# Optimization experiments

Hardware: AMD Instinct MI355X
Metric: run time of the kernel (lower is better)

Reference implementation:

```python
import jax, jax.numpy as jnp
import numpy as np

EPS = 1e-6


def setup_inputs() -> dict:
    key = jax.random.key(0)
    k1, k2 = jax.random.split(key)
    B, Lq, Lk, D = 16, 1024, 1024, 512
    query = jax.random.normal(k1, (B, Lq, D), dtype=jnp.float32)
    context = jax.random.normal(k2, (B, Lk, D), dtype=jnp.float32)
    gamma = jnp.ones((D,), dtype=jnp.float32)
    beta = jnp.zeros((D,), dtype=jnp.float32)
    return {"query": query, "context": context, "gamma": gamma, "beta": beta}


def _layer_norm(x, gamma, beta):
    mean = jnp.mean(x, axis=-1, keepdims=True)
    var = jnp.var(x, axis=-1, keepdims=True)
    return gamma * (x - mean) * jax.lax.rsqrt(var + EPS) + beta


def reference(query, context, gamma, beta):
    # query: [B, Lq, D], context: [B, Lk, D]
    D = query.shape[-1]
    scale = 1.0 / np.sqrt(D).astype(np.float32)
    # additive-style tanh-activated scores: [B, Lq, Lk]
    score = jnp.tanh(jnp.einsum('bqd,bkd->bqk', query, context) * scale)
    attn = jax.nn.softmax(score, axis=2)
    # dropout is identity in eval/reference mode
    out = jnp.einsum('bqk,bkd->bqd', attn, context)
    out = _layer_norm(out + query, gamma, beta)
    return out
```

## Files before the change

kernel.cpp:

```cpp
#include <hip/hip_runtime.h>
#include <hip/hip_bf16.h>
#include <cstdint>

#define LQ 1024
#define LK 1024
#define DD 512
#define NB 16
#define QB 64
#define KB 32
#define NT (LK / KB)
#define CSTRIDE 1088
#define CSZ (32 * CSTRIDE)
#define PSZ (64 * 80)

typedef short bf16x8 __attribute__((ext_vector_type(8)));
typedef float f32x4 __attribute__((ext_vector_type(4)));

__device__ __forceinline__ uint16_t f2bf(float f) {
  uint32_t u = __builtin_bit_cast(uint32_t, f);
  u = (u + 0x7fffu + ((u >> 16) & 1u)) >> 16;
  return (uint16_t)u;
}

__device__ __forceinline__ void load_lds16(const void* g, void* l) {
  __builtin_amdgcn_global_load_lds(
      (const __attribute__((address_space(1))) uint32_t*)g,
      (__attribute__((address_space(3))) uint32_t*)l, 16, 0, 0);
}

__global__ __launch_bounds__(256) void prep_kernel(const float* __restrict__ c,
                                                   uint16_t* __restrict__ cb,
                                                   uint16_t* __restrict__ ct) {
  __shared__ float t[32][33];
  const int k0 = blockIdx.x * 32, d0 = blockIdx.y * 32, b = blockIdx.z;
  const float* src = c + (size_t)b * LK * DD;
  uint16_t* cbd = cb + (size_t)b * LK * DD;
  uint16_t* ctd = ct + (size_t)b * DD * LK;
  const int tx = threadIdx.x, ty = threadIdx.y;
  for (int j = 0; j < 4; ++j) {
    int k = ty + j * 8;
    float v = src[(size_t)(k0 + k) * DD + d0 + tx];
    t[k][tx] = v;
    cbd[(size_t)(k0 + k) * DD + d0 + tx] = f2bf(v);
  }
  __syncthreads();
  for (int j = 0; j < 4; ++j) {
    int d = ty + j * 8;
    ctd[(size_t)(d0 + d) * LK + k0 + tx] = f2bf(t[tx][d]);
  }
}

__global__ __launch_bounds__(512, 2) void attn_kernel(
    const uint16_t* __restrict__ Cb, const uint16_t* __restrict__ Ctb,
    const float* __restrict__ Qf, const float* __restrict__ gamma,
    const float* __restrict__ beta, float* __restrict__ out) {
  __shared__ uint4 cs4[3 * CSZ / 16];
  __shared__ char plds[3 * PSZ];
  __shared__ float denom_s[64];
  __shared__ float rsum_s[64], rsumsq_s[64], mean_s[64], rstd_s[64];

  const int tid = threadIdx.x;
  const int w = tid >> 6, l = tid & 63, c = l & 15, g = l >> 4;
  const int orig = blockIdx.x;
  const int virt = ((orig & 7) << 5) | (orig >> 3);
  const int b = virt >> 4, qblk = virt & 15;
  const int q0 = qblk * QB;
  const int mt = w & 1, qt = w >> 1;
  const float scale = 0.044194173824159216f;

  if (tid < 64) { denom_s[tid] = 0.f; rsum_s[tid] = 0.f; rsumsq_s[tid] = 0.f; }

  bf16x8 qfrag[16];
  {
    const float* qrow = Qf + ((size_t)b * LQ + q0 + qt * 16 + c) * DD;
    for (int s = 0; s < 16; ++s) {
      float4 a0 = *(const float4*)(qrow + s * 32 + g * 8);
      float4 a1 = *(const float4*)(qrow + s * 32 + g * 8 + 4);
      ushort4 u0, u1;
      u0.x = f2bf(a0.x); u0.y = f2bf(a0.y); u0.z = f2bf(a0.z); u0.w = f2bf(a0.w);
      u1.x = f2bf(a1.x); u1.y = f2bf(a1.y); u1.z = f2bf(a1.z); u1.w = f2bf(a1.w);
      union { ushort4 u[2]; bf16x8 v; } pk;
      pk.u[0] = u0; pk.u[1] = u1;
      qfrag[s] = pk.v;
    }
  }

  const int kkA = mt * 16 + c;
  const int aoff = kkA * CSTRIDE + ((g ^ (kkA & 3)) * 16);

  f32x4 oacc[4][4];
  for (int i = 0; i < 4; ++i)
    for (int j = 0; j < 4; ++j) oacc[i][j] = (f32x4){0.f, 0.f, 0.f, 0.f};
  float dacc = 0.f;

  const char* cbyte = (const char*)Cb + (size_t)b * LK * DD * 2;
  const char* ctbyte = (const char*)Ctb + (size_t)b * DD * LK * 2;

  int csrcoff[4];
  for (int j = 0; j < 4; ++j) {
    int r = w * 4 + j;
    csrcoff[j] = r * 1024 + ((l * 16) ^ ((r & 3) << 4));
  }
  const char* pbbase = ctbyte + (size_t)(w * 64 + c) * 2048 + g * 16;

  char* cs0 = (char*)cs4;
  char* cs1 = cs0 + CSZ;
  char* cs2 = cs1 + CSZ;
  char* pl0 = plds;
  char* pl1 = pl0 + PSZ;
  char* pl2 = pl1 + PSZ;
  const int pwoff = (qt * 16 + c) * 80 + (mt * 16 + g * 4) * 2;
  const int proff = c * 80 + g * 16;

  auto stageC = [&](char* dst, int kt2) {
    const char* s0 = cbyte + (size_t)kt2 * 32768;
    for (int j = 0; j < 4; ++j)
      load_lds16(s0 + csrcoff[j], dst + (w * 4 + j) * CSTRIDE);
  };
  auto loadPB = [&](bf16x8(&pbn)[4], int kt2) {
    const char* p = pbbase + kt2 * 64;
    pbn[0] = *(const bf16x8*)(p);
    pbn[1] = *(const bf16x8*)(p + 32768);
    pbn[2] = *(const bf16x8*)(p + 65536);
    pbn[3] = *(const bf16x8*)(p + 98304);
  };

  bf16x8 pbX[4], pbY[4], pbZ[4];

  stageC(cs0, 0);
  stageC(cs1, 1);
  __syncthreads();

  auto body = [&](int kt, const char* csR, char* csW, const char* pR, char* pW,
                  bf16x8(&pbc)[4], bf16x8(&pbn)[4], bool doStage, bool doPV) {
    if (doStage) stageC(csW, kt + 2);
    loadPB(pbn, kt);
    if (doPV) {
      bf16x8 pa[4];
      for (int q2 = 0; q2 < 4; ++q2) pa[q2] = *(const bf16x8*)(pR + proff + q2 * 1280);
      __builtin_amdgcn_s_setprio(1);
      for (int q2 = 0; q2 < 4; ++q2)
        for (int n2 = 0; n2 < 4; ++n2)
          oacc[q2][n2] =
              __builtin_amdgcn_mfma_f32_16x16x32_bf16(pa[q2], pbc[n2], oacc[q2][n2], 0, 0, 0);
      __builtin_amdgcn_s_setprio(0);
    }
    f32x4 s0v = {0.f, 0.f, 0.f, 0.f}, s1v = {0.f, 0.f, 0.f, 0.f};
    {
      const char* ar = csR + aoff;
      __builtin_amdgcn_s_setprio(1);
      for (int s = 0; s < 8; ++s) {
        bf16x8 a0 = *(const bf16x8*)(ar + s * 64);
        bf16x8 a1 = *(const bf16x8*)(ar + (s + 8) * 64);
        s0v = __builtin_amdgcn_mfma_f32_16x16x32_bf16(a0, qfrag[s], s0v, 0, 0, 0);
        s1v = __builtin_amdgcn_mfma_f32_16x16x32_bf16(a1, qfrag[s + 8], s1v, 0, 0, 0);
      }
      __builtin_amdgcn_s_setprio(0);
    }
    {
      float pv[4];
      for (int i = 0; i < 4; ++i) {
        float sv = (s0v[i] + s1v[i]) * scale;
        float e2 = __expf(sv * 2.f);
        float r = __builtin_amdgcn_rcpf(e2 + 1.f);
        float th = (e2 - 1.f) * r;
        float p = __expf(th);
        pv[i] = p;
        dacc += p;
      }
      uint2 pk;
      pk.x = ((uint32_t)f2bf(pv[1]) << 16) | f2bf(pv[0]);
      pk.y = ((uint32_t)f2bf(pv[3]) << 16) | f2bf(pv[2]);
      *(uint2*)(pW + pwoff) = pk;
    }
    asm volatile("s_waitcnt lgkmcnt(0)" ::: "memory");
    __builtin_amdgcn_s_barrier();
    __builtin_amdgcn_sched_barrier(0);
  };

  for (int kt = 0; kt < NT - 2; kt += 3) {
    body(kt,     cs0, cs2, pl2, pl0, pbZ, pbX, kt + 2 < NT, kt > 0);
    body(kt + 1, cs1, cs0, pl0, pl1, pbX, pbY, kt + 3 < NT, true);
    body(kt + 2, cs2, cs1, pl1, pl2, pbY, pbZ, kt + 4 < NT, true);
  }
  body(NT - 2, cs0, cs2, pl2, pl0, pbZ, pbX, false, true);
  body(NT - 1, cs1, cs0, pl0, pl1, pbX, pbY, false, true);
  {
    bf16x8 pa[4];
    for (int q2 = 0; q2 < 4; ++q2) pa[q2] = *(const bf16x8*)(pl1 + proff + q2 * 1280);
    for (int q2 = 0; q2 < 4; ++q2)
      for (int n2 = 0; n2 < 4; ++n2)
        oacc[q2][n2] =
            __builtin_amdgcn_mfma_f32_16x16x32_bf16(pa[q2], pbY[n2], oacc[q2][n2], 0, 0, 0);
  }

  float dv = dacc;
  dv += __shfl_xor(dv, 16);
  dv += __shfl_xor(dv, 32);
  if (l < 16) atomicAdd(&denom_s[qt * 16 + l], dv);
  __syncthreads();

  const float* qsrc = Qf + ((size_t)b * LQ + q0) * DD;
  for (int q2 = 0; q2 < 4; ++q2)
    for (int i = 0; i < 4; ++i) {
      int row = q2 * 16 + g * 4 + i;
      float inv = 1.f / denom_s[row];
      for (int nt = 0; nt < 4; ++nt) {
        int d = w * 64 + nt * 16 + c;
        float o = oacc[q2][nt][i] * inv + qsrc[(size_t)row * DD + d];
        oacc[q2][nt][i] = o;
      }
    }
  for (int q2 = 0; q2 < 4; ++q2)
    for (int i = 0; i < 4; ++i) {
      float s1 = 0.f, s2 = 0.f;
      for (int nt = 0; nt < 4; ++nt) {
        float v = oacc[q2][nt][i];
        s1 += v;
        s2 += v * v;
      }
      s1 += __shfl_xor(s1, 1); s2 += __shfl_xor(s2, 1);
      s1 += __shfl_xor(s1, 2); s2 += __shfl_xor(s2, 2);
      s1 += __shfl_xor(s1, 4); s2 += __shfl_xor(s2, 4);
      s1 += __shfl_xor(s1, 8); s2 += __shfl_xor(s2, 8);
      if (c == 0) {
        int row = q2 * 16 + g * 4 + i;
        atomicAdd(&rsum_s[row], s1);
        atomicAdd(&rsumsq_s[row], s2);
      }
    }
  __syncthreads();
  if (tid < 64) {
    float m = rsum_s[tid] * (1.f / DD);
    float var = rsumsq_s[tid] * (1.f / DD) - m * m;
    mean_s[tid] = m;
    rstd_s[tid] = rsqrtf(fmaxf(var, 0.f) + 1e-6f);
  }
  __syncthreads();
  float* op = out + ((size_t)b * LQ + q0) * DD;
  for (int q2 = 0; q2 < 4; ++q2)
    for (int i = 0; i < 4; ++i) {
      int row = q2 * 16 + g * 4 + i;
      float m = mean_s[row], r = rstd_s[row];
      for (int nt = 0; nt < 4; ++nt) {
        int d = w * 64 + nt * 16 + c;
        op[(size_t)row * DD + d] = gamma[d] * ((oacc[q2][nt][i] - m) * r) + beta[d];
      }
    }
}

__global__ __launch_bounds__(256) void naive_kernel(const float* __restrict__ Q,
                                                    const float* __restrict__ C,
                                                    const float* __restrict__ gamma,
                                                    const float* __restrict__ beta,
                                                    float* __restrict__ out) {
  const int row = blockIdx.x;
  const int b = row >> 10;
  const int tid = threadIdx.x;
  __shared__ float qs[DD];
  __shared__ float ps[LK];
  __shared__ float ys[DD];
  __shared__ float red[256];
  const float* qp = Q + (size_t)row * DD;
  const float* cb = C + (size_t)b * LK * DD;
  for (int d = tid; d < DD; d += 256) qs[d] = qp[d];
  __syncthreads();
  for (int k = tid; k < LK; k += 256) {
    const float* cr = cb + (size_t)k * DD;
    float s = 0.f;
    for (int d = 0; d < DD; ++d) s += qs[d] * cr[d];
    s *= 0.044194173824159216f;
    float e2 = __expf(2.f * s);
    float th = (e2 - 1.f) / (e2 + 1.f);
    ps[k] = __expf(th);
  }
  __syncthreads();
  float dsum = 0.f;
  for (int k = tid; k < LK; k += 256) dsum += ps[k];
  red[tid] = dsum;
  __syncthreads();
  for (int off = 128; off; off >>= 1) {
    if (tid < off) red[tid] += red[tid + off];
    __syncthreads();
  }
  float inv = 1.f / red[0];
  __syncthreads();
  for (int d = tid; d < DD; d += 256) {
    float o = 0.f;
    for (int k = 0; k < LK; ++k) o += ps[k] * cb[(size_t)k * DD + d];
    ys[d] = o * inv + qs[d];
  }
  __syncthreads();
  float s1 = 0.f;
  for (int d = tid; d < DD; d += 256) s1 += ys[d];
  red[tid] = s1;
  __syncthreads();
  for (int off = 128; off; off >>= 1) {
    if (tid < off) red[tid] += red[tid + off];
    __syncthreads();
  }
  float mean = red[0] * (1.f / DD);
  __syncthreads();
  float s2 = 0.f;
  for (int d = tid; d < DD; d += 256) {
    float v = ys[d] - mean;
    s2 += v * v;
  }
  red[tid] = s2;
  __syncthreads();
  for (int off = 128; off; off >>= 1) {
    if (tid < off) red[tid] += red[tid + off];
    __syncthreads();
  }
  float rstd = rsqrtf(red[0] * (1.f / DD) + 1e-6f);
  for (int d = tid; d < DD; d += 256)
    out[(size_t)row * DD + d] = gamma[d] * ((ys[d] - mean) * rstd) + beta[d];
}

extern "C" void kernel_launch(void* const* d_in, const int* in_sizes, int n_in,
                              void* d_out, int out_size, void* d_ws, size_t ws_size,
                              hipStream_t stream) {
  const float* Qf = (const float*)d_in[0];
  const float* Cf = (const float*)d_in[1];
  const float* gamma = (const float*)d_in[2];
  const float* beta = (const float*)d_in[3];
  float* out = (float*)d_out;
  const size_t nelem = (size_t)NB * LK * DD;
  const size_t need = nelem * 2 * 2;
  if (ws_size >= need) {
    uint16_t* Cb = (uint16_t*)d_ws;
    uint16_t* Ctb = Cb + nelem;
    prep_kernel<<<dim3(LK / 32, DD / 32, NB), dim3(32, 8), 0, stream>>>(Cf, Cb, Ctb);
    attn_kernel<<<256, 512, 0, stream>>>(Cb, Ctb, Qf, gamma, beta, out);
  } else {
    naive_kernel<<<NB * LQ, 256, 0, stream>>>(Qf, Cf, gamma, beta, out);
  }
}
```

Before: 96.15 us.

## Halve query block to 32 rows with 256-thread blocks and double buffering

Cuts the query tile from 64 to 32 rows, uses 4 waves per block instead of 8, and launches 512 blocks instead of 256 so more of the chip's compute units get work. Each wave now owns 128 output columns, with 8 PV accumulators per query subtile. The C staging pipeline drops from triple to double buffering, and the hand-placed waitcnt plus barrier is replaced by __syncthreads. The cost is that each K/V tile is reused across half as many query rows, so global traffic for the context doubles, and the shallower pipeline may expose more load latency.

```diff
diff --git a/kernel.cpp b/kernel.cpp
--- a/kernel.cpp
+++ b/kernel.cpp
@@ -6,12 +6,12 @@
 #define LK 1024
 #define DD 512
 #define NB 16
-#define QB 64
+#define QB 32
 #define KB 32
 #define NT (LK / KB)
 #define CSTRIDE 1088
 #define CSZ (32 * CSTRIDE)
-#define PSZ (64 * 80)
+#define PSZ (QB * 80)
 
 typedef short bf16x8 __attribute__((ext_vector_type(8)));
 typedef float f32x4 __attribute__((ext_vector_type(4)));
@@ -50,25 +50,25 @@
   }
 }
 
-__global__ __launch_bounds__(512, 2) void attn_kernel(
+__global__ __launch_bounds__(256, 2) void attn_kernel(
     const uint16_t* __restrict__ Cb, const uint16_t* __restrict__ Ctb,
     const float* __restrict__ Qf, const float* __restrict__ gamma,
     const float* __restrict__ beta, float* __restrict__ out) {
-  __shared__ uint4 cs4[3 * CSZ / 16];
-  __shared__ char plds[3 * PSZ];
-  __shared__ float denom_s[64];
-  __shared__ float rsum_s[64], rsumsq_s[64], mean_s[64], rstd_s[64];
+  __shared__ uint4 cs4[2 * CSZ / 16];
+  __shared__ char plds[2 * PSZ];
+  __shared__ float denom_s[QB];
+  __shared__ float rsum_s[QB], rsumsq_s[QB], mean_s[QB], rstd_s[QB];
 
   const int tid = threadIdx.x;
   const int w = tid >> 6, l = tid & 63, c = l & 15, g = l >> 4;
   const int orig = blockIdx.x;
-  const int virt = ((orig & 7) << 5) | (orig >> 3);
-  const int b = virt >> 4, qblk = virt & 15;
+  const int virt = ((orig & 7) << 6) | (orig >> 3);
+  const int b = virt >> 5, qblk = virt & 31;
   const int q0 = qblk * QB;
   const int mt = w & 1, qt = w >> 1;
   const float scale = 0.044194173824159216f;
 
-  if (tid < 64) { denom_s[tid] = 0.f; rsum_s[tid] = 0.f; rsumsq_s[tid] = 0.f; }
+  if (tid < QB) { denom_s[tid] = 0.f; rsum_s[tid] = 0.f; rsumsq_s[tid] = 0.f; }
 
   bf16x8 qfrag[16];
   {
@@ -88,66 +88,63 @@
   const int kkA = mt * 16 + c;
   const int aoff = kkA * CSTRIDE + ((g ^ (kkA & 3)) * 16);
 
-  f32x4 oacc[4][4];
-  for (int i = 0; i < 4; ++i)
-    for (int j = 0; j < 4; ++j) oacc[i][j] = (f32x4){0.f, 0.f, 0.f, 0.f};
+  f32x4 oacc[2][8];
+  for (int i = 0; i < 2; ++i)
+    for (int j = 0; j < 8; ++j) oacc[i][j] = (f32x4){0.f, 0.f, 0.f, 0.f};
   float dacc = 0.f;
 
   const char* cbyte = (const char*)Cb + (size_t)b * LK * DD * 2;
   const char* ctbyte = (const char*)Ctb + (size_t)b * DD * LK * 2;
 
-  int csrcoff[4];
-  for (int j = 0; j < 4; ++j) {
-    int r = w * 4 + j;
+  int csrcoff[8];
+  for (int j = 0; j < 8; ++j) {
+    int r = w * 8 + j;
     csrcoff[j] = r * 1024 + ((l * 16) ^ ((r & 3) << 4));
   }
-  const char* pbbase = ctbyte + (size_t)(w * 64 + c) * 2048 + g * 16;
+  const char* pbbase = ctbyte + (size_t)(w * 128 + c) * 2048 + g * 16;
 
   char* cs0 = (char*)cs4;
   char* cs1 = cs0 + CSZ;
-  char* cs2 = cs1 + CSZ;
   char* pl0 = plds;
   char* pl1 = pl0 + PSZ;
-  char* pl2 = pl1 + PSZ;
   const int pwoff = (qt * 16 + c) * 80 + (mt * 16 + g * 4) * 2;
   const int proff = c * 80 + g * 16;
 
   auto stageC = [&](char* dst, int kt2) {
     const char* s0 = cbyte + (size_t)kt2 * 32768;
-    for (int j = 0; j < 4; ++j)
-      load_lds16(s0 + csrcoff[j], dst + (w * 4 + j) * CSTRIDE);
+    for (int j = 0; j < 8; ++j)
+      load_lds16(s0 + csrcoff[j], dst + (w * 8 + j) * CSTRIDE);
   };
-  auto loadPB = [&](bf16x8(&pbn)[4], int kt2) {
+  auto loadPB = [&](bf16x8(&pbn)[8], int kt2) {
     const char* p = pbbase + kt2 * 64;
-    pbn[0] = *(const bf16x8*)(p);
-    pbn[1] = *(const bf16x8*)(p + 32768);
-    pbn[2] = *(const bf16x8*)(p + 65536);
-    pbn[3] = *(const bf16x8*)(p + 98304);
+    for (int nt = 0; nt < 8; ++nt)
+      pbn[nt] = *(const bf16x8*)(p + (size_t)nt * 32768);
   };
 
-  bf16x8 pbX[4], pbY[4], pbZ[4];
+  bf16x8 pbA[8], pbB[8];
 
   stageC(cs0, 0);
-  stageC(cs1, 1);
-  __syncthreads();
-
-  auto body = [&](int kt, const char* csR, char* csW, const char* pR, char* pW,
-                  bf16x8(&pbc)[4], bf16x8(&pbn)[4], bool doStage, bool doPV) {
-    if (doStage) stageC(csW, kt + 2);
+  __syncthreads();
+
+  auto body = [&](int kt, bf16x8(&pbc)[8], bf16x8(&pbn)[8]) {
+    const int cur = kt & 1;
+    if (kt + 1 < NT) stageC(cur ? cs0 : cs1, kt + 1);
     loadPB(pbn, kt);
-    if (doPV) {
-      bf16x8 pa[4];
-      for (int q2 = 0; q2 < 4; ++q2) pa[q2] = *(const bf16x8*)(pR + proff + q2 * 1280);
+    if (kt) {
+      const char* par = (cur ? pl0 : pl1) + proff;
+      bf16x8 pa[2];
+      pa[0] = *(const bf16x8*)(par);
+      pa[1] = *(const bf16x8*)(par + 1280);
       __builtin_amdgcn_s_setprio(1);
-      for (int q2 = 0; q2 < 4; ++q2)
-        for (int n2 = 0; n2 < 4; ++n2)
+      for (int q2 = 0; q2 < 2; ++q2)
+        for (int n2 = 0; n2 < 8; ++n2)
           oacc[q2][n2] =
               __builtin_amdgcn_mfma_f32_16x16x32_bf16(pa[q2], pbc[n2], oacc[q2][n2], 0, 0, 0);
       __builtin_amdgcn_s_setprio(0);
     }
     f32x4 s0v = {0.f, 0.f, 0.f, 0.f}, s1v = {0.f, 0.f, 0.f, 0.f};
     {
-      const char* ar = csR + aoff;
+      const char* ar = (cur ? cs1 : cs0) + aoff;
       __builtin_amdgcn_s_setprio(1);
       for (int s = 0; s < 8; ++s) {
         bf16x8 a0 = *(const bf16x8*)(ar + s * 64);
@@ -171,27 +168,23 @@
       uint2 pk;
       pk.x = ((uint32_t)f2bf(pv[1]) << 16) | f2bf(pv[0]);
       pk.y = ((uint32_t)f2bf(pv[3]) << 16) | f2bf(pv[2]);
-      *(uint2*)(pW + pwoff) = pk;
-    }
-    asm volatile("s_waitcnt lgkmcnt(0)" ::: "memory");
-    __builtin_amdgcn_s_barrier();
-    __builtin_amdgcn_sched_barrier(0);
+      *(uint2*)((cur ? pl1 : pl0) + pwoff) = pk;
+    }
+    __syncthreads();
   };
 
-  for (int kt = 0; kt < NT - 2; kt += 3) {
-    body(kt,     cs0, cs2, pl2, pl0, pbZ, pbX, kt + 2 < NT, kt > 0);
-    body(kt + 1, cs1, cs0, pl0, pl1, pbX, pbY, kt + 3 < NT, true);
-    body(kt + 2, cs2, cs1, pl1, pl2, pbY, pbZ, kt + 4 < NT, true);
-  }
-  body(NT - 2, cs0, cs2, pl2, pl0, pbZ, pbX, false, true);
-  body(NT - 1, cs1, cs0, pl0, pl1, pbX, pbY, false, true);
+  for (int kt = 0; kt < NT; kt += 2) {
+    body(kt, pbB, pbA);
+    body(kt + 1, pbA, pbB);
+  }
   {
-    bf16x8 pa[4];
-    for (int q2 = 0; q2 < 4; ++q2) pa[q2] = *(const bf16x8*)(pl1 + proff + q2 * 1280);
-    for (int q2 = 0; q2 < 4; ++q2)
-      for (int n2 = 0; n2 < 4; ++n2)
+    bf16x8 pa[2];
+    pa[0] = *(const bf16x8*)(pl1 + proff);
+    pa[1] = *(const bf16x8*)(pl1 + proff + 1280);
+    for (int q2 = 0; q2 < 2; ++q2)
+      for (int n2 = 0; n2 < 8; ++n2)
         oacc[q2][n2] =
-            __builtin_amdgcn_mfma_f32_16x16x32_bf16(pa[q2], pbY[n2], oacc[q2][n2], 0, 0, 0);
+            __builtin_amdgcn_mfma_f32_16x16x32_bf16(pa[q2], pbB[n2], oacc[q2][n2], 0, 0, 0);
   }
 
   float dv = dacc;
@@ -201,20 +194,20 @@
   __syncthreads();
 
   const float* qsrc = Qf + ((size_t)b * LQ + q0) * DD;
-  for (int q2 = 0; q2 < 4; ++q2)
+  for (int q2 = 0; q2 < 2; ++q2)
     for (int i = 0; i < 4; ++i) {
       int row = q2 * 16 + g * 4 + i;
       float inv = 1.f / denom_s[row];
-      for (int nt = 0; nt < 4; ++nt) {
-        int d = w * 64 + nt * 16 + c;
+      for (int nt = 0; nt < 8; ++nt) {
+        int d = w * 128 + nt * 16 + c;
         float o = oacc[q2][nt][i] * inv + qsrc[(size_t)row * DD + d];
         oacc[q2][nt][i] = o;
       }
     }
-  for (int q2 = 0; q2 < 4; ++q2)
+  for (int q2 = 0; q2 < 2; ++q2)
     for (int i = 0; i < 4; ++i) {
       float s1 = 0.f, s2 = 0.f;
-      for (int nt = 0; nt < 4; ++nt) {
+      for (int nt = 0; nt < 8; ++nt) {
         float v = oacc[q2][nt][i];
         s1 += v;
         s2 += v * v;
@@ -230,7 +223,7 @@
       }
     }
   __syncthreads();
-  if (tid < 64) {
+  if (tid < QB) {
     float m = rsum_s[tid] * (1.f / DD);
     float var = rsumsq_s[tid] * (1.f / DD) - m * m;
     mean_s[tid] = m;
@@ -238,12 +231,12 @@
   }
   __syncthreads();
   float* op = out + ((size_t)b * LQ + q0) * DD;
-  for (int q2 = 0; q2 < 4; ++q2)
+  for (int q2 = 0; q2 < 2; ++q2)
     for (int i = 0; i < 4; ++i) {
       int row = q2 * 16 + g * 4 + i;
       float m = mean_s[row], r = rstd_s[row];
-      for (int nt = 0; nt < 4; ++nt) {
-        int d = w * 64 + nt * 16 + c;
+      for (int nt = 0; nt < 8; ++nt) {
+        int d = w * 128 + nt * 16 + c;
         op[(size_t)row * DD + d] = gamma[d] * ((oacc[q2][nt][i] - m) * r) + beta[d];
       }
     }
@@ -331,7 +324,7 @@
     uint16_t* Cb = (uint16_t*)d_ws;
     uint16_t* Ctb = Cb + nelem;
     prep_kernel<<<dim3(LK / 32, DD / 32, NB), dim3(32, 8), 0, stream>>>(Cf, Cb, Ctb);
-    attn_kernel<<<256, 512, 0, stream>>>(Cb, Ctb, Qf, gamma, beta, out);
+    attn_kernel<<<512, 256, 0, stream>>>(Cb, Ctb, Qf, gamma, beta, out);
   } else {
     naive_kernel<<<NB * LQ, 256, 0, stream>>>(Qf, Cf, gamma, beta, out);
   }
```

Result: slower. 109.7 us (+14.1%).

## Warp-specialize attention kernel into score and PV producer/consumer warp groups

Applied to the files above, without the earlier changes.

Splits the 512-thread block into a 1024-thread block. Waves 0-7 compute QK scores, tanh and exp and write P tiles to double-buffered LDS. Waves 8-15 stage C tiles into LDS, load transposed C, run the PV MFMAs and do the layernorm epilogue. The aim is to overlap score computation with the PV matmul and global loads across separate waves rather than interleaving both in every wave. In exchange, occupancy drops to one block per CU. The barrier pairing between the two groups is subtle and a possible correctness risk, including the matched __syncthreads counts and the vmcnt wait covering the staged loads.

```diff
diff --git a/kernel.cpp b/kernel.cpp
--- a/kernel.cpp
+++ b/kernel.cpp
@@ -11,7 +11,7 @@
 #define NT (LK / KB)
 #define CSTRIDE 1088
 #define CSZ (32 * CSTRIDE)
-#define PSZ (64 * 80)
+#define PSZ (QB * 80)
 
 typedef short bf16x8 __attribute__((ext_vector_type(8)));
 typedef float f32x4 __attribute__((ext_vector_type(4)));
@@ -50,14 +50,14 @@
   }
 }
 
-__global__ __launch_bounds__(512, 2) void attn_kernel(
+__global__ __launch_bounds__(1024) void attn_kernel(
     const uint16_t* __restrict__ Cb, const uint16_t* __restrict__ Ctb,
     const float* __restrict__ Qf, const float* __restrict__ gamma,
     const float* __restrict__ beta, float* __restrict__ out) {
   __shared__ uint4 cs4[3 * CSZ / 16];
-  __shared__ char plds[3 * PSZ];
-  __shared__ float denom_s[64];
-  __shared__ float rsum_s[64], rsumsq_s[64], mean_s[64], rstd_s[64];
+  __shared__ char plds[2 * PSZ];
+  __shared__ float denom_s[QB];
+  __shared__ float rsum_s[QB], rsumsq_s[QB], mean_s[QB], rstd_s[QB];
 
   const int tid = threadIdx.x;
   const int w = tid >> 6, l = tid & 63, c = l & 15, g = l >> 4;
@@ -65,89 +65,60 @@
   const int virt = ((orig & 7) << 5) | (orig >> 3);
   const int b = virt >> 4, qblk = virt & 15;
   const int q0 = qblk * QB;
-  const int mt = w & 1, qt = w >> 1;
   const float scale = 0.044194173824159216f;
 
-  if (tid < 64) { denom_s[tid] = 0.f; rsum_s[tid] = 0.f; rsumsq_s[tid] = 0.f; }
-
-  bf16x8 qfrag[16];
-  {
-    const float* qrow = Qf + ((size_t)b * LQ + q0 + qt * 16 + c) * DD;
-    for (int s = 0; s < 16; ++s) {
-      float4 a0 = *(const float4*)(qrow + s * 32 + g * 8);
-      float4 a1 = *(const float4*)(qrow + s * 32 + g * 8 + 4);
-      ushort4 u0, u1;
-      u0.x = f2bf(a0.x); u0.y = f2bf(a0.y); u0.z = f2bf(a0.z); u0.w = f2bf(a0.w);
-      u1.x = f2bf(a1.x); u1.y = f2bf(a1.y); u1.z = f2bf(a1.z); u1.w = f2bf(a1.w);
-      union { ushort4 u[2]; bf16x8 v; } pk;
-      pk.u[0] = u0; pk.u[1] = u1;
-      qfrag[s] = pk.v;
-    }
-  }
-
-  const int kkA = mt * 16 + c;
-  const int aoff = kkA * CSTRIDE + ((g ^ (kkA & 3)) * 16);
-
-  f32x4 oacc[4][4];
-  for (int i = 0; i < 4; ++i)
-    for (int j = 0; j < 4; ++j) oacc[i][j] = (f32x4){0.f, 0.f, 0.f, 0.f};
-  float dacc = 0.f;
+  if (tid < QB) { denom_s[tid] = 0.f; rsum_s[tid] = 0.f; rsumsq_s[tid] = 0.f; }
 
   const char* cbyte = (const char*)Cb + (size_t)b * LK * DD * 2;
   const char* ctbyte = (const char*)Ctb + (size_t)b * DD * LK * 2;
-
-  int csrcoff[4];
-  for (int j = 0; j < 4; ++j) {
-    int r = w * 4 + j;
-    csrcoff[j] = r * 1024 + ((l * 16) ^ ((r & 3) << 4));
-  }
-  const char* pbbase = ctbyte + (size_t)(w * 64 + c) * 2048 + g * 16;
-
   char* cs0 = (char*)cs4;
   char* cs1 = cs0 + CSZ;
   char* cs2 = cs1 + CSZ;
   char* pl0 = plds;
-  char* pl1 = pl0 + PSZ;
-  char* pl2 = pl1 + PSZ;
-  const int pwoff = (qt * 16 + c) * 80 + (mt * 16 + g * 4) * 2;
-  const int proff = c * 80 + g * 16;
-
-  auto stageC = [&](char* dst, int kt2) {
-    const char* s0 = cbyte + (size_t)kt2 * 32768;
-    for (int j = 0; j < 4; ++j)
-      load_lds16(s0 + csrcoff[j], dst + (w * 4 + j) * CSTRIDE);
-  };
-  auto loadPB = [&](bf16x8(&pbn)[4], int kt2) {
-    const char* p = pbbase + kt2 * 64;
-    pbn[0] = *(const bf16x8*)(p);
-    pbn[1] = *(const bf16x8*)(p + 32768);
-    pbn[2] = *(const bf16x8*)(p + 65536);
-    pbn[3] = *(const bf16x8*)(p + 98304);
-  };
-
-  bf16x8 pbX[4], pbY[4], pbZ[4];
-
-  stageC(cs0, 0);
-  stageC(cs1, 1);
-  __syncthreads();
-
-  auto body = [&](int kt, const char* csR, char* csW, const char* pR, char* pW,
-                  bf16x8(&pbc)[4], bf16x8(&pbn)[4], bool doStage, bool doPV) {
-    if (doStage) stageC(csW, kt + 2);
-    loadPB(pbn, kt);
-    if (doPV) {
-      bf16x8 pa[4];
-      for (int q2 = 0; q2 < 4; ++q2) pa[q2] = *(const bf16x8*)(pR + proff + q2 * 1280);
-      __builtin_amdgcn_s_setprio(1);
-      for (int q2 = 0; q2 < 4; ++q2)
-        for (int n2 = 0; n2 < 4; ++n2)
-          oacc[q2][n2] =
-              __builtin_amdgcn_mfma_f32_16x16x32_bf16(pa[q2], pbc[n2], oacc[q2][n2], 0, 0, 0);
-      __builtin_amdgcn_s_setprio(0);
-    }
-    f32x4 s0v = {0.f, 0.f, 0.f, 0.f}, s1v = {0.f, 0.f, 0.f, 0.f};
+  char* pl1 = plds + PSZ;
+
+  const int cw = w - 8;
+  int csrcoff[4];
+  for (int j = 0; j < 4; ++j) {
+    int r = (cw & 7) * 4 + j;
+    csrcoff[j] = r * 1024 + ((l * 16) ^ ((r & 3) << 4));
+  }
+
+  if (w >= 8) {
+    const char* s0 = cbyte;
+    for (int j = 0; j < 4; ++j) {
+      load_lds16(s0 + csrcoff[j], cs0 + (cw * 4 + j) * CSTRIDE);
+      load_lds16(s0 + 32768 + csrcoff[j], cs1 + (cw * 4 + j) * CSTRIDE);
+    }
+  }
+  __syncthreads();
+
+  if (w < 8) {
+    const int mt = w & 1, qt = w >> 1;
+    bf16x8 qfrag[16];
     {
+      const float* qrow = Qf + ((size_t)b * LQ + q0 + qt * 16 + c) * DD;
+      for (int s = 0; s < 16; ++s) {
+        float4 a0 = *(const float4*)(qrow + s * 32 + g * 8);
+        float4 a1 = *(const float4*)(qrow + s * 32 + g * 8 + 4);
+        ushort4 u0, u1;
+        u0.x = f2bf(a0.x); u0.y = f2bf(a0.y); u0.z = f2bf(a0.z); u0.w = f2bf(a0.w);
+        u1.x = f2bf(a1.x); u1.y = f2bf(a1.y); u1.z = f2bf(a1.z); u1.w = f2bf(a1.w);
+        union { ushort4 u[2]; bf16x8 v; } pk;
+        pk.u[0] = u0; pk.u[1] = u1;
+        qfrag[s] = pk.v;
+      }
+    }
+    const int kkA = mt * 16 + c;
+    const int aoff = kkA * CSTRIDE + ((g ^ (kkA & 3)) * 16);
+    const int pwoff = (qt * 16 + c) * 80 + (mt * 16 + g * 4) * 2;
+    float dacc = 0.f;
+
+#pragma unroll
+    for (int kt = 0; kt < NT; ++kt) {
+      const char* csR = (kt % 3 == 0) ? cs0 : (kt % 3 == 1) ? cs1 : cs2;
       const char* ar = csR + aoff;
+      f32x4 s0v = {0.f, 0.f, 0.f, 0.f}, s1v = {0.f, 0.f, 0.f, 0.f};
       __builtin_amdgcn_s_setprio(1);
       for (int s = 0; s < 8; ++s) {
         bf16x8 a0 = *(const bf16x8*)(ar + s * 64);
@@ -156,8 +127,6 @@
         s1v = __builtin_amdgcn_mfma_f32_16x16x32_bf16(a1, qfrag[s + 8], s1v, 0, 0, 0);
       }
       __builtin_amdgcn_s_setprio(0);
-    }
-    {
       float pv[4];
       for (int i = 0; i < 4; ++i) {
         float sv = (s0v[i] + s1v[i]) * scale;
@@ -171,82 +140,122 @@
       uint2 pk;
       pk.x = ((uint32_t)f2bf(pv[1]) << 16) | f2bf(pv[0]);
       pk.y = ((uint32_t)f2bf(pv[3]) << 16) | f2bf(pv[2]);
-      *(uint2*)(pW + pwoff) = pk;
-    }
-    asm volatile("s_waitcnt lgkmcnt(0)" ::: "memory");
-    __builtin_amdgcn_s_barrier();
-    __builtin_amdgcn_sched_barrier(0);
-  };
-
-  for (int kt = 0; kt < NT - 2; kt += 3) {
-    body(kt,     cs0, cs2, pl2, pl0, pbZ, pbX, kt + 2 < NT, kt > 0);
-    body(kt + 1, cs1, cs0, pl0, pl1, pbX, pbY, kt + 3 < NT, true);
-    body(kt + 2, cs2, cs1, pl1, pl2, pbY, pbZ, kt + 4 < NT, true);
-  }
-  body(NT - 2, cs0, cs2, pl2, pl0, pbZ, pbX, false, true);
-  body(NT - 1, cs1, cs0, pl0, pl1, pbX, pbY, false, true);
-  {
-    bf16x8 pa[4];
-    for (int q2 = 0; q2 < 4; ++q2) pa[q2] = *(const bf16x8*)(pl1 + proff + q2 * 1280);
+      *(uint2*)(((kt & 1) ? pl1 : pl0) + pwoff) = pk;
+      asm volatile("s_waitcnt lgkmcnt(0)" ::: "memory");
+      __builtin_amdgcn_s_barrier();
+      __builtin_amdgcn_sched_barrier(0);
+    }
+    float dv = dacc;
+    dv += __shfl_xor(dv, 16);
+    dv += __shfl_xor(dv, 32);
+    if (l < 16) atomicAdd(&denom_s[qt * 16 + l], dv);
+  } else {
+    const char* pbbase = ctbyte + (size_t)(cw * 64 + c) * 2048 + g * 16;
+    const int proff = c * 80 + g * 16;
+    f32x4 oacc[4][4];
+    for (int i = 0; i < 4; ++i)
+      for (int j = 0; j < 4; ++j) oacc[i][j] = (f32x4){0.f, 0.f, 0.f, 0.f};
+    bf16x8 pb[4];
+
+#pragma unroll
+    for (int kt = 0; kt < NT; ++kt) {
+      if (kt > 0) {
+        const char* p = pbbase + (size_t)(kt - 1) * 64;
+        pb[0] = *(const bf16x8*)(p);
+        pb[1] = *(const bf16x8*)(p + 32768);
+        pb[2] = *(const bf16x8*)(p + 65536);
+        pb[3] = *(const bf16x8*)(p + 98304);
+      }
+      __builtin_amdgcn_sched_barrier(0);
+      if (kt + 2 < NT) {
+        char* csW = ((kt + 2) % 3 == 0) ? cs0 : ((kt + 2) % 3 == 1) ? cs1 : cs2;
+        const char* s0 = cbyte + (size_t)(kt + 2) * 32768;
+        for (int j = 0; j < 4; ++j)
+          load_lds16(s0 + csrcoff[j], csW + (cw * 4 + j) * CSTRIDE);
+      }
+      if (kt > 0) {
+        const char* par = ((kt & 1) ? pl0 : pl1) + proff;
+        bf16x8 pa[4];
+        for (int q2 = 0; q2 < 4; ++q2) pa[q2] = *(const bf16x8*)(par + q2 * 1280);
+        __builtin_amdgcn_s_setprio(1);
+        for (int q2 = 0; q2 < 4; ++q2)
+          for (int n2 = 0; n2 < 4; ++n2)
+            oacc[q2][n2] =
+                __builtin_amdgcn_mfma_f32_16x16x32_bf16(pa[q2], pb[n2], oacc[q2][n2], 0, 0, 0);
+        __builtin_amdgcn_s_setprio(0);
+      }
+      asm volatile("s_waitcnt vmcnt(8)" ::: "memory");
+      __builtin_amdgcn_s_barrier();
+      __builtin_amdgcn_sched_barrier(0);
+    }
+    {
+      const char* p = pbbase + (size_t)(NT - 1) * 64;
+      pb[0] = *(const bf16x8*)(p);
+      pb[1] = *(const bf16x8*)(p + 32768);
+      pb[2] = *(const bf16x8*)(p + 65536);
+      pb[3] = *(const bf16x8*)(p + 98304);
+      const char* par = pl1 + proff;
+      bf16x8 pa[4];
+      for (int q2 = 0; q2 < 4; ++q2) pa[q2] = *(const bf16x8*)(par + q2 * 1280);
+      for (int q2 = 0; q2 < 4; ++q2)
+        for (int n2 = 0; n2 < 4; ++n2)
+          oacc[q2][n2] =
+              __builtin_amdgcn_mfma_f32_16x16x32_bf16(pa[q2], pb[n2], oacc[q2][n2], 0, 0, 0);
+    }
+    __syncthreads();
+
+    const float* qsrc = Qf + ((size_t)b * LQ + q0) * DD;
     for (int q2 = 0; q2 < 4; ++q2)
-      for (int n2 = 0; n2 < 4; ++n2)
-        oacc[q2][n2] =
-            __builtin_amdgcn_mfma_f32_16x16x32_bf16(pa[q2], pbY[n2], oacc[q2][n2], 0, 0, 0);
-  }
-
-  float dv = dacc;
-  dv += __shfl_xor(dv, 16);
-  dv += __shfl_xor(dv, 32);
-  if (l < 16) atomicAdd(&denom_s[qt * 16 + l], dv);
-  __syncthreads();
-
-  const float* qsrc = Qf + ((size_t)b * LQ + q0) * DD;
-  for (int q2 = 0; q2 < 4; ++q2)
-    for (int i = 0; i < 4; ++i) {
-      int row = q2 * 16 + g * 4 + i;
-      float inv = 1.f / denom_s[row];
-      for (int nt = 0; nt < 4; ++nt) {
-        int d = w * 64 + nt * 16 + c;
-        float o = oacc[q2][nt][i] * inv + qsrc[(size_t)row * DD + d];
-        oacc[q2][nt][i] = o;
-      }
-    }
-  for (int q2 = 0; q2 < 4; ++q2)
-    for (int i = 0; i < 4; ++i) {
-      float s1 = 0.f, s2 = 0.f;
-      for (int nt = 0; nt < 4; ++nt) {
-        float v = oacc[q2][nt][i];
-        s1 += v;
-        s2 += v * v;
-      }
-      s1 += __shfl_xor(s1, 1); s2 += __shfl_xor(s2, 1);
-      s1 += __shfl_xor(s1, 2); s2 += __shfl_xor(s2, 2);
-      s1 += __shfl_xor(s1, 4); s2 += __shfl_xor(s2, 4);
-      s1 += __shfl_xor(s1, 8); s2 += __shfl_xor(s2, 8);
-      if (c == 0) {
+      for (int i = 0; i < 4; ++i) {
         int row = q2 * 16 + g * 4 + i;
-        atomicAdd(&rsum_s[row], s1);
-        atomicAdd(&rsumsq_s[row], s2);
-      }
-    }
-  __syncthreads();
-  if (tid < 64) {
+        float inv = 1.f / denom_s[row];
+        for (int nt = 0; nt < 4; ++nt) {
+          int d = cw * 64 + nt * 16 + c;
+          float o = oacc[q2][nt][i] * inv + qsrc[(size_t)row * DD + d];
+          oacc[q2][nt][i] = o;
+        }
+      }
+    for (int q2 = 0; q2 < 4; ++q2)
+      for (int i = 0; i < 4; ++i) {
+        float s1 = 0.f, s2 = 0.f;
+        for (int nt = 0; nt < 4; ++nt) {
+          float v = oacc[q2][nt][i];
+          s1 += v;
+          s2 += v * v;
+        }
+        s1 += __shfl_xor(s1, 1); s2 += __shfl_xor(s2, 1);
+        s1 += __shfl_xor(s1, 2); s2 += __shfl_xor(s2, 2);
+        s1 += __shfl_xor(s1, 4); s2 += __shfl_xor(s2, 4);
+        s1 += __shfl_xor(s1, 8); s2 += __shfl_xor(s2, 8);
+        if (c == 0) {
+          int row = q2 * 16 + g * 4 + i;
+          atomicAdd(&rsum_s[row], s1);
+          atomicAdd(&rsumsq_s[row], s2);
+        }
+      }
+    __syncthreads();
+    __syncthreads();
+    float* op = out + ((size_t)b * LQ + q0) * DD;
+    for (int q2 = 0; q2 < 4; ++q2)
+      for (int i = 0; i < 4; ++i) {
+        int row = q2 * 16 + g * 4 + i;
+        float m = mean_s[row], r = rstd_s[row];
+        for (int nt = 0; nt < 4; ++nt) {
+          int d = cw * 64 + nt * 16 + c;
+          op[(size_t)row * DD + d] = gamma[d] * ((oacc[q2][nt][i] - m) * r) + beta[d];
+        }
+      }
+    return;
+  }
+  __syncthreads();
+  __syncthreads();
+  if (tid < QB) {
     float m = rsum_s[tid] * (1.f / DD);
     float var = rsumsq_s[tid] * (1.f / DD) - m * m;
     mean_s[tid] = m;
     rstd_s[tid] = rsqrtf(fmaxf(var, 0.f) + 1e-6f);
   }
   __syncthreads();
-  float* op = out + ((size_t)b * LQ + q0) * DD;
-  for (int q2 = 0; q2 < 4; ++q2)
-    for (int i = 0; i < 4; ++i) {
-      int row = q2 * 16 + g * 4 + i;
-      float m = mean_s[row], r = rstd_s[row];
-      for (int nt = 0; nt < 4; ++nt) {
-        int d = w * 64 + nt * 16 + c;
-        op[(size_t)row * DD + d] = gamma[d] * ((oacc[q2][nt][i] - m) * r) + beta[d];
-      }
-    }
 }
 
 __global__ __launch_bounds__(256) void naive_kernel(const float* __restrict__ Q,
@@ -331,7 +340,7 @@
     uint16_t* Cb = (uint16_t*)d_ws;
     uint16_t* Ctb = Cb + nelem;
     prep_kernel<<<dim3(LK / 32, DD / 32, NB), dim3(32, 8), 0, stream>>>(Cf, Cb, Ctb);
-    attn_kernel<<<256, 512, 0, stream>>>(Cb, Ctb, Qf, gamma, beta, out);
+    attn_kernel<<<256, 1024, 0, stream>>>(Cb, Ctb, Qf, gamma, beta, out);
   } else {
     naive_kernel<<<NB * LQ, 256, 0, stream>>>(Qf, Cf, gamma, beta, out);
   }
```

New measurement: 100.9 us. 1.05x slower.

## Replace triple-buffered skewed pipeline with double-buffered two-barrier loop

Applied to the files above, without the earlier changes.

Replaces the 3-stage rotating LDS pipeline, where the P·V MFMA for tile kt-1 overlapped the score MFMA for tile kt, with a 2-buffer scheme. Each iteration computes scores, writes P to one LDS buffer, synchronizes, then does P·V in the same step, prefetching the next C tile and Ct fragments one step ahead. This cuts LDS usage, which may help occupancy, and registers for the extra PB buffer. In exchange it adds a second barrier per tile and loses the cross-tile overlap of the two MFMA phases.

```diff
diff --git a/kernel.cpp b/kernel.cpp
--- a/kernel.cpp
+++ b/kernel.cpp
@@ -11,7 +11,7 @@
 #define NT (LK / KB)
 #define CSTRIDE 1088
 #define CSZ (32 * CSTRIDE)
-#define PSZ (64 * 80)
+#define PSZ (QB * 80)
 
 typedef short bf16x8 __attribute__((ext_vector_type(8)));
 typedef float f32x4 __attribute__((ext_vector_type(4)));
@@ -54,10 +54,10 @@
     const uint16_t* __restrict__ Cb, const uint16_t* __restrict__ Ctb,
     const float* __restrict__ Qf, const float* __restrict__ gamma,
     const float* __restrict__ beta, float* __restrict__ out) {
-  __shared__ uint4 cs4[3 * CSZ / 16];
-  __shared__ char plds[3 * PSZ];
-  __shared__ float denom_s[64];
-  __shared__ float rsum_s[64], rsumsq_s[64], mean_s[64], rstd_s[64];
+  __shared__ uint4 cs4[2 * CSZ / 16];
+  __shared__ char plds[PSZ];
+  __shared__ float denom_s[QB];
+  __shared__ float rsum_s[QB], rsumsq_s[QB], mean_s[QB], rstd_s[QB];
 
   const int tid = threadIdx.x;
   const int w = tid >> 6, l = tid & 63, c = l & 15, g = l >> 4;
@@ -68,7 +68,7 @@
   const int mt = w & 1, qt = w >> 1;
   const float scale = 0.044194173824159216f;
 
-  if (tid < 64) { denom_s[tid] = 0.f; rsum_s[tid] = 0.f; rsumsq_s[tid] = 0.f; }
+  if (tid < QB) { denom_s[tid] = 0.f; rsum_s[tid] = 0.f; rsumsq_s[tid] = 0.f; }
 
   bf16x8 qfrag[16];
   {
@@ -105,10 +105,6 @@
 
   char* cs0 = (char*)cs4;
   char* cs1 = cs0 + CSZ;
-  char* cs2 = cs1 + CSZ;
-  char* pl0 = plds;
-  char* pl1 = pl0 + PSZ;
-  char* pl2 = pl1 + PSZ;
   const int pwoff = (qt * 16 + c) * 80 + (mt * 16 + g * 4) * 2;
   const int proff = c * 80 + g * 16;
 
@@ -118,32 +114,26 @@
       load_lds16(s0 + csrcoff[j], dst + (w * 4 + j) * CSTRIDE);
   };
   auto loadPB = [&](bf16x8(&pbn)[4], int kt2) {
-    const char* p = pbbase + kt2 * 64;
+    const char* p = pbbase + (size_t)kt2 * 64;
     pbn[0] = *(const bf16x8*)(p);
     pbn[1] = *(const bf16x8*)(p + 32768);
     pbn[2] = *(const bf16x8*)(p + 65536);
     pbn[3] = *(const bf16x8*)(p + 98304);
   };
 
-  bf16x8 pbX[4], pbY[4], pbZ[4];
+  bf16x8 pbA[4], pbB[4];
 
   stageC(cs0, 0);
-  stageC(cs1, 1);
-  __syncthreads();
-
-  auto body = [&](int kt, const char* csR, char* csW, const char* pR, char* pW,
-                  bf16x8(&pbc)[4], bf16x8(&pbn)[4], bool doStage, bool doPV) {
-    if (doStage) stageC(csW, kt + 2);
-    loadPB(pbn, kt);
-    if (doPV) {
-      bf16x8 pa[4];
-      for (int q2 = 0; q2 < 4; ++q2) pa[q2] = *(const bf16x8*)(pR + proff + q2 * 1280);
-      __builtin_amdgcn_s_setprio(1);
-      for (int q2 = 0; q2 < 4; ++q2)
-        for (int n2 = 0; n2 < 4; ++n2)
-          oacc[q2][n2] =
-              __builtin_amdgcn_mfma_f32_16x16x32_bf16(pa[q2], pbc[n2], oacc[q2][n2], 0, 0, 0);
-      __builtin_amdgcn_s_setprio(0);
+  loadPB(pbA, 0);
+  asm volatile("s_waitcnt vmcnt(4) lgkmcnt(0)" ::: "memory");
+  __builtin_amdgcn_s_barrier();
+  __builtin_amdgcn_sched_barrier(0);
+
+  auto body = [&](int kt, const char* csR, char* csW, bf16x8(&pbc)[4],
+                  bf16x8(&pbn)[4], bool hasNext) {
+    if (hasNext) {
+      stageC(csW, kt + 1);
+      loadPB(pbn, kt + 1);
     }
     f32x4 s0v = {0.f, 0.f, 0.f, 0.f}, s1v = {0.f, 0.f, 0.f, 0.f};
     {
@@ -171,27 +161,32 @@
       uint2 pk;
       pk.x = ((uint32_t)f2bf(pv[1]) << 16) | f2bf(pv[0]);
       pk.y = ((uint32_t)f2bf(pv[3]) << 16) | f2bf(pv[2]);
-      *(uint2*)(pW + pwoff) = pk;
+      *(uint2*)(plds + pwoff) = pk;
     }
     asm volatile("s_waitcnt lgkmcnt(0)" ::: "memory");
     __builtin_amdgcn_s_barrier();
     __builtin_amdgcn_sched_barrier(0);
+    {
+      bf16x8 pa[4];
+      for (int q2 = 0; q2 < 4; ++q2) pa[q2] = *(const bf16x8*)(plds + proff + q2 * 1280);
+      __builtin_amdgcn_s_setprio(1);
+      for (int q2 = 0; q2 < 4; ++q2)
+        for (int n2 = 0; n2 < 4; ++n2)
+          oacc[q2][n2] =
+              __builtin_amdgcn_mfma_f32_16x16x32_bf16(pa[q2], pbc[n2], oacc[q2][n2], 0, 0, 0);
+      __builtin_amdgcn_s_setprio(0);
+    }
+    if (hasNext)
+      asm volatile("s_waitcnt vmcnt(4) lgkmcnt(0)" ::: "memory");
+    else
+      asm volatile("s_waitcnt lgkmcnt(0)" ::: "memory");
+    __builtin_amdgcn_s_barrier();
+    __builtin_amdgcn_sched_barrier(0);
   };
 
-  for (int kt = 0; kt < NT - 2; kt += 3) {
-    body(kt,     cs0, cs2, pl2, pl0, pbZ, pbX, kt + 2 < NT, kt > 0);
-    body(kt + 1, cs1, cs0, pl0, pl1, pbX, pbY, kt + 3 < NT, true);
-    body(kt + 2, cs2, cs1, pl1, pl2, pbY, pbZ, kt + 4 < NT, true);
-  }
-  body(NT - 2, cs0, cs2, pl2, pl0, pbZ, pbX, false, true);
-  body(NT - 1, cs1, cs0, pl0, pl1, pbX, pbY, false, true);
-  {
-    bf16x8 pa[4];
-    for (int q2 = 0; q2 < 4; ++q2) pa[q2] = *(const bf16x8*)(pl1 + proff + q2 * 1280);
-    for (int q2 = 0; q2 < 4; ++q2)
-      for (int n2 = 0; n2 < 4; ++n2)
-        oacc[q2][n2] =
-            __builtin_amdgcn_mfma_f32_16x16x32_bf16(pa[q2], pbY[n2], oacc[q2][n2], 0, 0, 0);
+  for (int kt = 0; kt < NT; kt += 2) {
+    body(kt, cs0, cs1, pbA, pbB, true);
+    body(kt + 1, cs1, cs0, pbB, pbA, kt + 2 < NT);
   }
 
   float dv = dacc;
@@ -230,7 +225,7 @@
       }
     }
   __syncthreads();
-  if (tid < 64) {
+  if (tid < QB) {
     float m = rsum_s[tid] * (1.f / DD);
     float var = rsumsq_s[tid] * (1.f / DD) - m * m;
     mean_s[tid] = m;
```

Result: slower. 105.7 us (+9.9%).
